# Optimization experiments

Measured on AMD Instinct MI355X. Metric: run time of the kernel, lower is better.

Reference implementation:

```python
import jax, jax.numpy as jnp
import numpy as np

LN_EPS = 1e-6


def setup_inputs() -> dict:
    key = jax.random.key(0)
    ks = jax.random.split(key, 10)
    B, S, D, M, P = 64, 512, 1024, 512, 3
    seq_out = jax.random.normal(ks[0], (B, S, D), dtype=jnp.float32)
    # dependency-tree style adjacency: sparse 0/1, stored dense as in the module
    adj = (jax.random.uniform(ks[1], (B, S, S)) < 0.02).astype(jnp.float32)
    aspect_mask = jax.random.randint(ks[2], (B, S), 0, 2, dtype=jnp.int32)
    # guarantee at least one aspect token per row (asp_wn divisor)
    aspect_mask = aspect_mask.at[:, 0].set(1)
    sc = 0.02
    return {
        "seq_out": seq_out,
        "adj": adj,
        "aspect_mask": aspect_mask,
        "ln_a": jnp.ones((D,), jnp.float32),
        "ln_b": jnp.zeros((D,), jnp.float32),
        "asp_w": jax.random.normal(ks[3], (D,), jnp.float32) * sc,
        "asp_b": jnp.zeros((), jnp.float32),
        "W0": jax.random.normal(ks[4], (D, M), jnp.float32) * sc,
        "b0": jnp.zeros((M,), jnp.float32),
        "W1": jax.random.normal(ks[5], (M, M), jnp.float32) * sc,
        "b1": jnp.zeros((M,), jnp.float32),
        "W2": jax.random.normal(ks[6], (M, M), jnp.float32) * sc,
        "b2": jnp.zeros((M,), jnp.float32),
        "cls_w": jax.random.normal(ks[7], (2 * M, P), jnp.float32) * sc,
        "cls_b": jnp.zeros((P,), jnp.float32),
    }


def _torch_layernorm(x, a, b):
    # torch code: a*(x-mean)/(std+eps)+b with unbiased std (Bessel, /(D-1))
    D = x.shape[-1]
    mean = jnp.mean(x, axis=-1, keepdims=True)
    xc = x - mean
    std = jnp.sqrt(jnp.sum(xc * xc, axis=-1, keepdims=True) / (D - 1))
    return a * xc / (std + LN_EPS) + b


def reference(seq_out, adj, aspect_mask, ln_a, ln_b, asp_w, asp_b,
              W0, b0, W1, b1, W2, b2, cls_w, cls_b):
    tgt = aspect_mask.astype(seq_out.dtype)                 # [B,S] labels == BCE weight (eval mode)
    x = _torch_layernorm(seq_out, ln_a, ln_b)               # [B,S,D]

    # aspect classification head + weighted BCEWithLogits (mean over all elems)
    z = jnp.einsum('bsd,d->bs', x, asp_w) + asp_b           # logits [B,S]
    bce = jnp.logaddexp(0.0, z) - z * tgt                   # stable BCE-with-logits
    loss_asp = jnp.mean(tgt * bce)
    aspect_pred = jax.nn.sigmoid(z)

    # dense-adjacency GCN (dropout = identity in eval)
    denom = jnp.sum(adj, axis=2, keepdims=True) + 1.0       # [B,S,1]
    out = x
    for W, b in ((W0, b0), (W1, b1), (W2, b2)):
        Ax = jnp.einsum('bst,btd->bsd', adj, out)           # aggregate
        out = jax.nn.relu((Ax @ W + b) / denom)             # project + degree-norm + relu

    # aspect-masked mean pool + global mean pool
    asp_wn = jnp.sum(tgt, axis=1, keepdims=True)            # [B,1]
    dep = jnp.einsum('bsm,bs->bm', out, tgt) / asp_wn       # [B,M]
    glob = jnp.mean(out, axis=1)                            # [B,M]

    feature = jnp.concatenate([dep, glob], axis=-1) @ cls_w + cls_b
    logits = jax.nn.softmax(feature, axis=1)
    return feature, logits, aspect_pred, loss_asp
```

## Files before the change

kernel.cpp:

```cpp
#include <hip/hip_runtime.h>
#include <math.h>

typedef __bf16 bf16;
typedef bf16 bf16x2 __attribute__((ext_vector_type(2)));
typedef bf16 bf16x4 __attribute__((ext_vector_type(4)));
typedef bf16 bf16x8 __attribute__((ext_vector_type(8)));
typedef float f32x4 __attribute__((ext_vector_type(4)));

#define NROWS 32768
#define DDIM 1024
#define MDIM 512

__device__ __forceinline__ float wave_reduce_sum(float v) {
#pragma unroll
  for (int o = 32; o > 0; o >>= 1) v += __shfl_down(v, o, 64);
  return v;
}
__device__ __forceinline__ float wave_allreduce_sum(float v) {
#pragma unroll
  for (int o = 32; o > 0; o >>= 1) v += __shfl_xor(v, o, 64);
  return v;
}

__device__ __forceinline__ void load_lds16(const bf16* g, bf16* l) {
  __builtin_amdgcn_global_load_lds(
      (const __attribute__((address_space(1))) unsigned int*)g,
      (__attribute__((address_space(3))) unsigned int*)l, 16, 0, 0);
}

__global__ __launch_bounds__(256) void prep_kernel(
    const float* __restrict__ seq, const float* __restrict__ adj,
    const int* __restrict__ amask, const float* __restrict__ ga,
    const float* __restrict__ gb, const float* __restrict__ aw,
    const float* __restrict__ ab, const float* __restrict__ W0,
    const float* __restrict__ W1, const float* __restrict__ W2,
    bf16* __restrict__ xn, float* __restrict__ aspect_pred,
    float* __restrict__ loss_arr, unsigned short* __restrict__ nbr,
    int* __restrict__ cnt, float* __restrict__ denomv,
    bf16* __restrict__ W0T, bf16* __restrict__ W1T, bf16* __restrict__ W2T) {
  const int bid = blockIdx.x;
  const int tid = threadIdx.x;
  const int lane = tid & 63;
  const int wv = tid >> 6;

  if (bid < 8192) {
    const int row = bid * 4 + wv;
    const float* xr = seq + (size_t)row * DDIM;
    float4 v[4];
    float s = 0.0f, sq = 0.0f;
#pragma unroll
    for (int j = 0; j < 4; ++j) {
      v[j] = *(const float4*)&xr[j * 256 + lane * 4];
      s += v[j].x + v[j].y + v[j].z + v[j].w;
      sq += v[j].x * v[j].x + v[j].y * v[j].y + v[j].z * v[j].z + v[j].w * v[j].w;
    }
    s = wave_allreduce_sum(s);
    sq = wave_allreduce_sum(sq);
    float mean = s * (1.0f / 1024.0f);
    float var = (sq - 1024.0f * mean * mean) * (1.0f / 1023.0f);
    var = fmaxf(var, 0.0f);
    float inv = 1.0f / (sqrtf(var) + 1e-6f);
    float zp = 0.0f;
#pragma unroll
    for (int j = 0; j < 4; ++j) {
      int c = j * 256 + lane * 4;
      float4 a4 = *(const float4*)&ga[c];
      float4 b4 = *(const float4*)&gb[c];
      float4 w4 = *(const float4*)&aw[c];
      float x0 = a4.x * (v[j].x - mean) * inv + b4.x;
      float x1 = a4.y * (v[j].y - mean) * inv + b4.y;
      float x2 = a4.z * (v[j].z - mean) * inv + b4.z;
      float x3 = a4.w * (v[j].w - mean) * inv + b4.w;
      bf16x4 o;
      o[0] = (bf16)x0; o[1] = (bf16)x1; o[2] = (bf16)x2; o[3] = (bf16)x3;
      *(bf16x4*)&xn[(size_t)row * DDIM + c] = o;
      zp += x0 * w4.x + x1 * w4.y + x2 * w4.z + x3 * w4.w;
    }
    zp = wave_reduce_sum(zp);
    if (lane == 0) {
      float z = zp + ab[0];
      aspect_pred[row] = 1.0f / (1.0f + expf(-z));
      float tgt = (float)amask[row];
      float bce = fmaxf(z, 0.0f) + log1pf(expf(-fabsf(z))) - z * tgt;
      loss_arr[row] = tgt * bce;
    }
  } else if (bid < 16384) {
    const int row = (bid - 8192) * 4 + wv;
    const float* ar = adj + (size_t)row * 512;
    unsigned short* nr = nbr + (size_t)row * 512;
    unsigned long long below = (1ull << lane) - 1ull;
    int base = 0;
#pragma unroll
    for (int t = 0; t < 2; ++t) {
      float4 v = *(const float4*)&ar[t * 256 + lane * 4];
      unsigned long long m0 = __ballot(v.x != 0.0f);
      unsigned long long m1 = __ballot(v.y != 0.0f);
      unsigned long long m2 = __ballot(v.z != 0.0f);
      unsigned long long m3 = __ballot(v.w != 0.0f);
      int c0 = __popcll(m0), c1 = __popcll(m1), c2 = __popcll(m2);
      int col = t * 256 + lane * 4;
      if (v.x != 0.0f) nr[base + __popcll(m0 & below)] = (unsigned short)(col + 0);
      if (v.y != 0.0f) nr[base + c0 + __popcll(m1 & below)] = (unsigned short)(col + 1);
      if (v.z != 0.0f) nr[base + c0 + c1 + __popcll(m2 & below)] = (unsigned short)(col + 2);
      if (v.w != 0.0f) nr[base + c0 + c1 + c2 + __popcll(m3 & below)] = (unsigned short)(col + 3);
      base += c0 + c1 + c2 + __popcll(m3);
    }
    if (lane == 0) { cnt[row] = base; denomv[row] = (float)base + 1.0f; }
  } else {
    int e = ((bid - 16384) * 256 + tid) * 4;
    if (e < 524288) {
      float4 v = *(const float4*)&W0[e];
      int k = e >> 9, n = e & 511;
      W0T[(size_t)(n + 0) * 1024 + k] = (bf16)v.x;
      W0T[(size_t)(n + 1) * 1024 + k] = (bf16)v.y;
      W0T[(size_t)(n + 2) * 1024 + k] = (bf16)v.z;
      W0T[(size_t)(n + 3) * 1024 + k] = (bf16)v.w;
    } else if (e < 786432) {
      int e2 = e - 524288;
      float4 v = *(const float4*)&W1[e2];
      int k = e2 >> 9, n = e2 & 511;
      W1T[(size_t)(n + 0) * 512 + k] = (bf16)v.x;
      W1T[(size_t)(n + 1) * 512 + k] = (bf16)v.y;
      W1T[(size_t)(n + 2) * 512 + k] = (bf16)v.z;
      W1T[(size_t)(n + 3) * 512 + k] = (bf16)v.w;
    } else {
      int e3 = e - 786432;
      float4 v = *(const float4*)&W2[e3];
      int k = e3 >> 9, n = e3 & 511;
      W2T[(size_t)(n + 0) * 512 + k] = (bf16)v.x;
      W2T[(size_t)(n + 1) * 512 + k] = (bf16)v.y;
      W2T[(size_t)(n + 2) * 512 + k] = (bf16)v.z;
      W2T[(size_t)(n + 3) * 512 + k] = (bf16)v.w;
    }
  }
}

#define BAR  __builtin_amdgcn_s_barrier()
#define WAITL do { asm volatile("s_waitcnt lgkmcnt(0)" ::: "memory"); \
                   __builtin_amdgcn_sched_barrier(0); } while (0)
#define WAITV4 do { asm volatile("s_waitcnt vmcnt(4)" ::: "memory"); \
                    __builtin_amdgcn_sched_barrier(0); } while (0)

__global__ __launch_bounds__(512, 2) void gemm256(const bf16* __restrict__ A,
                                                  const bf16* __restrict__ BT,
                                                  bf16* __restrict__ C,
                                                  int K) {
  __shared__ __align__(16) bf16 SMEM[65536];
  bf16 (*As)[16384] = (bf16(*)[16384])SMEM;
  bf16 (*Bs)[16384] = (bf16(*)[16384])(SMEM + 32768);
  const int tid = threadIdx.x;
  const int lane = tid & 63;
  const int wave = tid >> 6;
  const int wr = wave >> 2;
  const int wc = wave & 3;
  const int T = K >> 6;

  const int p = blockIdx.x;
  const int chunk = gridDim.x >> 3;
  const int wg = (p & 7) * chunk + (p >> 3);
  const int m0 = (wg >> 1) * 256;
  const int n0 = (wg & 1) * 256;

  const int srow = tid >> 3;
  const int scol8 = (tid & 7) ^ (srow & 7);

#define STAGEA(t, h)                                                          \
  do {                                                                        \
    int kt_ = ((t) < T) ? (t) * 64 : 0;                                       \
    const bf16* s_ = A + (size_t)(m0 + (h) * 128 + srow) * K + kt_ + scol8*8; \
    bf16* d_ = &As[(t) & 1][(h) * 8192 + wave * 512];                         \
    load_lds16(s_, d_);                                                       \
    load_lds16(s_ + (size_t)64 * K, d_ + 4096);                               \
  } while (0)
#define STAGEB(t, h)                                                          \
  do {                                                                        \
    int kt_ = ((t) < T) ? (t) * 64 : 0;                                       \
    const bf16* s_ = BT + (size_t)(n0 + (h) * 128 + srow) * K + kt_ + scol8*8;\
    bf16* d_ = &Bs[(t) & 1][(h) * 8192 + wave * 512];                         \
    load_lds16(s_, d_);                                                       \
    load_lds16(s_ + (size_t)64 * K, d_ + 4096);                               \
  } while (0)

  const int abase = (wr * 128 + (lane & 15)) * 64 + (lane >> 4) * 8;
  const int bbase = (wc * 64 + (lane & 15)) * 64 + (lane >> 4) * 8;
  const int axor = (lane & 7) << 3;

  bf16x8 areg[4][2], breg[4][2];
  f32x4 acc[8][4];
#pragma unroll
  for (int i = 0; i < 8; ++i)
#pragma unroll
    for (int j = 0; j < 4; ++j)
#pragma unroll
      for (int r = 0; r < 4; ++r) acc[i][j][r] = 0.0f;

#define LDA(buf_, qm)                                                         \
  _Pragma("unroll") for (int i_ = 0; i_ < 4; ++i_)                            \
  _Pragma("unroll") for (int h2_ = 0; h2_ < 2; ++h2_)                         \
    areg[i_][h2_] = *(const bf16x8*)&As[buf_][                                \
        (abase + ((qm)*4 + i_) * 1024 + h2_ * 32) ^ axor];
#define LDB(buf_, qn)                                                         \
  _Pragma("unroll") for (int j_ = 0; j_ < 2; ++j_)                            \
  _Pragma("unroll") for (int h2_ = 0; h2_ < 2; ++h2_)                         \
    breg[(qn)*2 + j_][h2_] = *(const bf16x8*)&Bs[buf_][                       \
        (bbase + ((qn)*2 + j_) * 1024 + h2_ * 32) ^ axor];
#define MFMAQ(qm, qn)                                                         \
  __builtin_amdgcn_s_setprio(1);                                              \
  _Pragma("unroll") for (int i_ = 0; i_ < 4; ++i_)                            \
  _Pragma("unroll") for (int j_ = 0; j_ < 2; ++j_)                            \
  _Pragma("unroll") for (int h2_ = 0; h2_ < 2; ++h2_)                         \
    acc[(qm)*4 + i_][(qn)*2 + j_] = __builtin_amdgcn_mfma_f32_16x16x32_bf16(  \
        areg[i_][h2_], breg[(qn)*2 + j_][h2_], acc[(qm)*4 + i_][(qn)*2 + j_], \
        0, 0, 0);                                                             \
  __builtin_amdgcn_s_setprio(0);

  STAGEA(0, 0); STAGEA(0, 1); STAGEB(0, 0); STAGEB(0, 1);
  STAGEB(1, 0); STAGEB(1, 1);
  WAITV4;
  BAR;

  const int NIT = T >> 1;
  for (int it = 0; it < NIT; ++it) {
    const int t1 = 2 * it + 1, t2 = 2 * it + 2, t3 = 2 * it + 3;
    LDA(0, 0); LDB(0, 0); STAGEA(t1, 0);
    BAR; WAITL; MFMAQ(0, 0); BAR;
    LDB(0, 1); STAGEA(t1, 1);
    BAR; WAITL; MFMAQ(0, 1); BAR;
    LDA(0, 1); STAGEB(t2, 0);
    BAR; WAITL; MFMAQ(1, 0); BAR;
    STAGEB(t2, 1);
    BAR; WAITL; MFMAQ(1, 1); WAITV4; BAR;
    LDA(1, 0); LDB(1, 0); STAGEA(t2, 0);
    BAR; WAITL; MFMAQ(0, 0); BAR;
    LDB(1, 1); STAGEA(t2, 1);
    BAR; WAITL; MFMAQ(0, 1); BAR;
    LDA(1, 1); STAGEB(t3, 0);
    BAR; WAITL; MFMAQ(1, 0); BAR;
    STAGEB(t3, 1);
    BAR; WAITL; MFMAQ(1, 1); WAITV4; BAR;
  }

  const int cn = lane & 15;
  const int rb = (lane >> 4) * 4;
#pragma unroll
  for (int i = 0; i < 8; ++i)
#pragma unroll
    for (int j = 0; j < 4; ++j) {
      int row = wr * 128 + i * 16 + rb;
      int colb = wc * 64 + j * 16 + cn;
#pragma unroll
      for (int r = 0; r < 4; ++r)
        SMEM[((row + r) << 8) + (colb ^ (((row + r) & 7) << 4))] =
            (bf16)acc[i][j][r];
    }
  __syncthreads();
  const size_t cbase = (size_t)m0 * MDIM + n0;
#pragma unroll
  for (int q = 0; q < 16; ++q) {
    int e = q * 4096 + tid * 8;
    int row = e >> 8, col = e & 255;
    *(bf16x8*)&C[cbase + (size_t)row * MDIM + col] =
        *(const bf16x8*)&SMEM[(row << 8) + (col ^ ((row & 7) << 4))];
  }
}

__global__ __launch_bounds__(128) void agg_kernel(const bf16* __restrict__ P,
                                                  const unsigned short* __restrict__ nbr,
                                                  const int* __restrict__ cnt,
                                                  const float* __restrict__ denomv,
                                                  const float* __restrict__ bias,
                                                  bf16* __restrict__ outb) {
  int p = blockIdx.x;
  int row = (p & 7) * 4096 + (p >> 3);
  int tid = threadIdx.x;
  int b = row >> 9;
  __shared__ unsigned short nl[512];
  int n = cnt[row];
  for (int i = tid; i < n; i += 128) nl[i] = nbr[(size_t)row * 512 + i];
  __syncthreads();
  const bf16* Pb = P + ((size_t)(b << 9)) * MDIM;
  int col = tid * 4;
  float a0 = 0, a1 = 0, a2 = 0, a3 = 0;
  for (int e = 0; e < n; ++e) {
    bf16x4 v = *(const bf16x4*)&Pb[(size_t)nl[e] * MDIM + col];
    a0 += (float)v[0]; a1 += (float)v[1]; a2 += (float)v[2]; a3 += (float)v[3];
  }
  float inv = 1.0f / denomv[row];
  float4 bb = *(const float4*)&bias[col];
  bf16x4 o;
  o[0] = (bf16)fmaxf((a0 + bb.x) * inv, 0.0f);
  o[1] = (bf16)fmaxf((a1 + bb.y) * inv, 0.0f);
  o[2] = (bf16)fmaxf((a2 + bb.z) * inv, 0.0f);
  o[3] = (bf16)fmaxf((a3 + bb.w) * inv, 0.0f);
  *(bf16x4*)&outb[(size_t)row * MDIM + col] = o;
}

__global__ __launch_bounds__(256) void pool_part(const bf16* __restrict__ outb,
                                                 const int* __restrict__ amask,
                                                 float* __restrict__ part) {
  int b = blockIdx.x >> 3;
  int slab = blockIdx.x & 7;
  int tid = threadIdx.x;
  int c0 = tid * 2;
  const bf16* ob = outb + (size_t)(b * 512 + slab * 64) * MDIM + c0;
  const int* am = amask + b * 512 + slab * 64;
  float a0 = 0, a1 = 0, t0 = 0, t1 = 0;
#pragma unroll 4
  for (int s = 0; s < 64; ++s) {
    bf16x2 v = *(const bf16x2*)&ob[(size_t)s * MDIM];
    float tg = (float)am[s];
    float v0 = (float)v[0], v1 = (float)v[1];
    a0 += v0; a1 += v1; t0 += v0 * tg; t1 += v1 * tg;
  }
  float* pp = part + ((size_t)blockIdx.x) * 1024;
  pp[c0] = t0; pp[c0 + 1] = t1;
  pp[512 + c0] = a0; pp[512 + c0 + 1] = a1;
}

__global__ __launch_bounds__(512) void poolcls_kernel(
    const float* __restrict__ part, const int* __restrict__ amask,
    const float* __restrict__ loss_arr, const float* __restrict__ cw,
    const float* __restrict__ cb, float* __restrict__ outp) {
  __shared__ float tg[512];
  __shared__ float shr[3][8];
  const int tid = threadIdx.x;
  const int b = blockIdx.x;

  if (b == 64) {
    float s = 0.0f;
    for (int i = tid; i < NROWS; i += 512) s += loss_arr[i];
    s = wave_reduce_sum(s);
    if ((tid & 63) == 0) shr[0][tid >> 6] = s;
    __syncthreads();
    if (tid == 0) {
      float t = 0.0f;
#pragma unroll
      for (int k = 0; k < 8; ++k) t += shr[0][k];
      outp[33152] = t * (1.0f / 32768.0f);
    }
    return;
  }

  tg[tid] = (float)amask[b * 512 + tid];
  __syncthreads();
  float wn = 0.0f;
#pragma unroll 8
  for (int s = 0; s < 512; ++s) wn += tg[s];
  float t = 0.0f, a = 0.0f;
  const float* pp = part + (size_t)b * 8 * 1024;
#pragma unroll
  for (int k = 0; k < 8; ++k) {
    t += pp[k * 1024 + tid];
    a += pp[k * 1024 + 512 + tid];
  }
  float f1 = t / wn;
  float f2 = a * (1.0f / 512.0f);

  float p0 = f1 * cw[tid * 3 + 0] + f2 * cw[(512 + tid) * 3 + 0];
  float p1 = f1 * cw[tid * 3 + 1] + f2 * cw[(512 + tid) * 3 + 1];
  float p2 = f1 * cw[tid * 3 + 2] + f2 * cw[(512 + tid) * 3 + 2];
  p0 = wave_reduce_sum(p0);
  p1 = wave_reduce_sum(p1);
  p2 = wave_reduce_sum(p2);
  if ((tid & 63) == 0) {
    shr[0][tid >> 6] = p0; shr[1][tid >> 6] = p1; shr[2][tid >> 6] = p2;
  }
  __syncthreads();
  if (tid == 0) {
    float q0 = 0, q1 = 0, q2 = 0;
#pragma unroll
    for (int k = 0; k < 8; ++k) { q0 += shr[0][k]; q1 += shr[1][k]; q2 += shr[2][k]; }
    q0 += cb[0]; q1 += cb[1]; q2 += cb[2];
    outp[b * 3 + 0] = q0;
    outp[b * 3 + 1] = q1;
    outp[b * 3 + 2] = q2;
    float m = fmaxf(q0, fmaxf(q1, q2));
    float e0 = expf(q0 - m), e1 = expf(q1 - m), e2 = expf(q2 - m);
    float inv = 1.0f / (e0 + e1 + e2);
    outp[192 + b * 3 + 0] = e0 * inv;
    outp[192 + b * 3 + 1] = e1 * inv;
    outp[192 + b * 3 + 2] = e2 * inv;
  }
}

extern "C" void kernel_launch(void* const* d_in, const int* in_sizes, int n_in,
                              void* d_out, int out_size, void* d_ws, size_t ws_size,
                              hipStream_t stream) {
  const float* seq   = (const float*)d_in[0];
  const float* adj   = (const float*)d_in[1];
  const int*   amask = (const int*)d_in[2];
  const float* ln_a  = (const float*)d_in[3];
  const float* ln_b  = (const float*)d_in[4];
  const float* asp_w = (const float*)d_in[5];
  const float* asp_b = (const float*)d_in[6];
  const float* W0    = (const float*)d_in[7];
  const float* b0    = (const float*)d_in[8];
  const float* W1    = (const float*)d_in[9];
  const float* b1    = (const float*)d_in[10];
  const float* W2    = (const float*)d_in[11];
  const float* b2    = (const float*)d_in[12];
  const float* cls_w = (const float*)d_in[13];
  const float* cls_b = (const float*)d_in[14];
  float* out = (float*)d_out;

  char* w = (char*)d_ws;
  bf16* P             = (bf16*)w;           w += (size_t)NROWS * MDIM * 2;
  bf16* xn            = (bf16*)w;           w += (size_t)NROWS * DDIM * 2;
  bf16* outb          = (bf16*)w;           w += (size_t)NROWS * MDIM * 2;
  unsigned short* nbr = (unsigned short*)w; w += (size_t)NROWS * 512 * 2;
  int* cnt            = (int*)w;            w += (size_t)NROWS * 4;
  float* denomv       = (float*)w;          w += (size_t)NROWS * 4;
  float* loss_arr     = (float*)w;          w += (size_t)NROWS * 4;
  float* part         = (float*)w;          w += (size_t)512 * 1024 * 4;
  bf16* W0T           = (bf16*)w;           w += (size_t)512 * 1024 * 2;
  bf16* W1T           = (bf16*)w;           w += (size_t)512 * 512 * 2;
  bf16* W2T           = (bf16*)w;           w += (size_t)512 * 512 * 2;

  prep_kernel<<<17408, 256, 0, stream>>>(seq, adj, amask, ln_a, ln_b, asp_w,
                                         asp_b, W0, W1, W2, xn, out + 384,
                                         loss_arr, nbr, cnt, denomv, W0T, W1T,
                                         W2T);
  gemm256<<<256, 512, 0, stream>>>(xn, W0T, P, 1024);
  agg_kernel<<<NROWS, 128, 0, stream>>>(P, nbr, cnt, denomv, b0, outb);
  gemm256<<<256, 512, 0, stream>>>(outb, W1T, P, 512);
  agg_kernel<<<NROWS, 128, 0, stream>>>(P, nbr, cnt, denomv, b1, outb);
  gemm256<<<256, 512, 0, stream>>>(outb, W2T, P, 512);
  agg_kernel<<<NROWS, 128, 0, stream>>>(P, nbr, cnt, denomv, b2, outb);
  pool_part<<<512, 256, 0, stream>>>(outb, amask, part);
  poolcls_kernel<<<65, 512, 0, stream>>>(part, amask, loss_arr, cls_w, cls_b,
                                         out);
}
```

Baseline: 266.0 us.

## Process eight rows per wave in prep kernel with prefetch; drop LDS staging in aggregation

```diff
diff --git a/kernel.cpp b/kernel.cpp
--- a/kernel.cpp
+++ b/kernel.cpp
@@ -43,94 +43,129 @@
   const int lane = tid & 63;
   const int wv = tid >> 6;
 
-  if (bid < 8192) {
-    const int row = bid * 4 + wv;
-    const float* xr = seq + (size_t)row * DDIM;
-    float4 v[4];
-    float s = 0.0f, sq = 0.0f;
-#pragma unroll
-    for (int j = 0; j < 4; ++j) {
-      v[j] = *(const float4*)&xr[j * 256 + lane * 4];
-      s += v[j].x + v[j].y + v[j].z + v[j].w;
-      sq += v[j].x * v[j].x + v[j].y * v[j].y + v[j].z * v[j].z + v[j].w * v[j].w;
-    }
-    s = wave_allreduce_sum(s);
-    sq = wave_allreduce_sum(sq);
-    float mean = s * (1.0f / 1024.0f);
-    float var = (sq - 1024.0f * mean * mean) * (1.0f / 1023.0f);
-    var = fmaxf(var, 0.0f);
-    float inv = 1.0f / (sqrtf(var) + 1e-6f);
-    float zp = 0.0f;
+  if (bid < 1024) {
+    const int row0 = (bid * 4 + wv) * 8;
+    float4 pa[4], pb[4], pw[4];
 #pragma unroll
     for (int j = 0; j < 4; ++j) {
       int c = j * 256 + lane * 4;
-      float4 a4 = *(const float4*)&ga[c];
-      float4 b4 = *(const float4*)&gb[c];
-      float4 w4 = *(const float4*)&aw[c];
-      float x0 = a4.x * (v[j].x - mean) * inv + b4.x;
-      float x1 = a4.y * (v[j].y - mean) * inv + b4.y;
-      float x2 = a4.z * (v[j].z - mean) * inv + b4.z;
-      float x3 = a4.w * (v[j].w - mean) * inv + b4.w;
-      bf16x4 o;
-      o[0] = (bf16)x0; o[1] = (bf16)x1; o[2] = (bf16)x2; o[3] = (bf16)x3;
-      *(bf16x4*)&xn[(size_t)row * DDIM + c] = o;
-      zp += x0 * w4.x + x1 * w4.y + x2 * w4.z + x3 * w4.w;
-    }
-    zp = wave_reduce_sum(zp);
-    if (lane == 0) {
-      float z = zp + ab[0];
-      aspect_pred[row] = 1.0f / (1.0f + expf(-z));
-      float tgt = (float)amask[row];
-      float bce = fmaxf(z, 0.0f) + log1pf(expf(-fabsf(z))) - z * tgt;
-      loss_arr[row] = tgt * bce;
-    }
-  } else if (bid < 16384) {
-    const int row = (bid - 8192) * 4 + wv;
-    const float* ar = adj + (size_t)row * 512;
-    unsigned short* nr = nbr + (size_t)row * 512;
-    unsigned long long below = (1ull << lane) - 1ull;
-    int base = 0;
-#pragma unroll
-    for (int t = 0; t < 2; ++t) {
-      float4 v = *(const float4*)&ar[t * 256 + lane * 4];
-      unsigned long long m0 = __ballot(v.x != 0.0f);
-      unsigned long long m1 = __ballot(v.y != 0.0f);
-      unsigned long long m2 = __ballot(v.z != 0.0f);
-      unsigned long long m3 = __ballot(v.w != 0.0f);
-      int c0 = __popcll(m0), c1 = __popcll(m1), c2 = __popcll(m2);
-      int col = t * 256 + lane * 4;
-      if (v.x != 0.0f) nr[base + __popcll(m0 & below)] = (unsigned short)(col + 0);
-      if (v.y != 0.0f) nr[base + c0 + __popcll(m1 & below)] = (unsigned short)(col + 1);
-      if (v.z != 0.0f) nr[base + c0 + c1 + __popcll(m2 & below)] = (unsigned short)(col + 2);
-      if (v.w != 0.0f) nr[base + c0 + c1 + c2 + __popcll(m3 & below)] = (unsigned short)(col + 3);
-      base += c0 + c1 + c2 + __popcll(m3);
-    }
-    if (lane == 0) { cnt[row] = base; denomv[row] = (float)base + 1.0f; }
+      pa[j] = *(const float4*)&ga[c];
+      pb[j] = *(const float4*)&gb[c];
+      pw[j] = *(const float4*)&aw[c];
+    }
+    const float ab0 = ab[0];
+    float4 v[4], vn[4];
+    {
+      const float* xr = seq + (size_t)row0 * DDIM;
+#pragma unroll
+      for (int j = 0; j < 4; ++j) vn[j] = *(const float4*)&xr[j * 256 + lane * 4];
+    }
+    for (int i = 0; i < 8; ++i) {
+      const int row = row0 + i;
+#pragma unroll
+      for (int j = 0; j < 4; ++j) v[j] = vn[j];
+      if (i < 7) {
+        const float* xr = seq + (size_t)(row + 1) * DDIM;
+#pragma unroll
+        for (int j = 0; j < 4; ++j) vn[j] = *(const float4*)&xr[j * 256 + lane * 4];
+      }
+      float s = 0.0f, sq = 0.0f;
+#pragma unroll
+      for (int j = 0; j < 4; ++j) {
+        s += v[j].x + v[j].y + v[j].z + v[j].w;
+        sq += v[j].x * v[j].x + v[j].y * v[j].y + v[j].z * v[j].z + v[j].w * v[j].w;
+      }
+      s = wave_allreduce_sum(s);
+      sq = wave_allreduce_sum(sq);
+      float mean = s * (1.0f / 1024.0f);
+      float var = (sq - 1024.0f * mean * mean) * (1.0f / 1023.0f);
+      var = fmaxf(var, 0.0f);
+      float inv = 1.0f / (sqrtf(var) + 1e-6f);
+      float zp = 0.0f;
+#pragma unroll
+      for (int j = 0; j < 4; ++j) {
+        float x0 = pa[j].x * (v[j].x - mean) * inv + pb[j].x;
+        float x1 = pa[j].y * (v[j].y - mean) * inv + pb[j].y;
+        float x2 = pa[j].z * (v[j].z - mean) * inv + pb[j].z;
+        float x3 = pa[j].w * (v[j].w - mean) * inv + pb[j].w;
+        bf16x4 o;
+        o[0] = (bf16)x0; o[1] = (bf16)x1; o[2] = (bf16)x2; o[3] = (bf16)x3;
+        *(bf16x4*)&xn[(size_t)row * DDIM + j * 256 + lane * 4] = o;
+        zp += x0 * pw[j].x + x1 * pw[j].y + x2 * pw[j].z + x3 * pw[j].w;
+      }
+      zp = wave_reduce_sum(zp);
+      if (lane == 0) {
+        float z = zp + ab0;
+        aspect_pred[row] = 1.0f / (1.0f + expf(-z));
+        float tgt = (float)amask[row];
+        float bce = fmaxf(z, 0.0f) + log1pf(expf(-fabsf(z))) - z * tgt;
+        loss_arr[row] = tgt * bce;
+      }
+    }
+  } else if (bid < 2048) {
+    const int row0 = ((bid - 1024) * 4 + wv) * 8;
+    const unsigned long long below = (1ull << lane) - 1ull;
+    float4 a0, a1, a0n, a1n;
+    {
+      const float* ar = adj + (size_t)row0 * 512;
+      a0n = *(const float4*)&ar[lane * 4];
+      a1n = *(const float4*)&ar[256 + lane * 4];
+    }
+    for (int i = 0; i < 8; ++i) {
+      const int row = row0 + i;
+      a0 = a0n; a1 = a1n;
+      if (i < 7) {
+        const float* ar = adj + (size_t)(row + 1) * 512;
+        a0n = *(const float4*)&ar[lane * 4];
+        a1n = *(const float4*)&ar[256 + lane * 4];
+      }
+      unsigned short* nr = nbr + (size_t)row * 512;
+      int base = 0;
+#pragma unroll
+      for (int t = 0; t < 2; ++t) {
+        float4 vv = t ? a1 : a0;
+        unsigned long long m0 = __ballot(vv.x != 0.0f);
+        unsigned long long m1 = __ballot(vv.y != 0.0f);
+        unsigned long long m2 = __ballot(vv.z != 0.0f);
+        unsigned long long m3 = __ballot(vv.w != 0.0f);
+        int c0 = __popcll(m0), c1 = __popcll(m1), c2 = __popcll(m2);
+        int col = t * 256 + lane * 4;
+        if (vv.x != 0.0f) nr[base + __popcll(m0 & below)] = (unsigned short)(col + 0);
+        if (vv.y != 0.0f) nr[base + c0 + __popcll(m1 & below)] = (unsigned short)(col + 1);
+        if (vv.z != 0.0f) nr[base + c0 + c1 + __popcll(m2 & below)] = (unsigned short)(col + 2);
+        if (vv.w != 0.0f) nr[base + c0 + c1 + c2 + __popcll(m3 & below)] = (unsigned short)(col + 3);
+        base += c0 + c1 + c2 + __popcll(m3);
+      }
+      if (lane == 0) { cnt[row] = base; denomv[row] = (float)base + 1.0f; }
+    }
   } else {
-    int e = ((bid - 16384) * 256 + tid) * 4;
-    if (e < 524288) {
-      float4 v = *(const float4*)&W0[e];
-      int k = e >> 9, n = e & 511;
-      W0T[(size_t)(n + 0) * 1024 + k] = (bf16)v.x;
-      W0T[(size_t)(n + 1) * 1024 + k] = (bf16)v.y;
-      W0T[(size_t)(n + 2) * 1024 + k] = (bf16)v.z;
-      W0T[(size_t)(n + 3) * 1024 + k] = (bf16)v.w;
-    } else if (e < 786432) {
-      int e2 = e - 524288;
-      float4 v = *(const float4*)&W1[e2];
-      int k = e2 >> 9, n = e2 & 511;
-      W1T[(size_t)(n + 0) * 512 + k] = (bf16)v.x;
-      W1T[(size_t)(n + 1) * 512 + k] = (bf16)v.y;
-      W1T[(size_t)(n + 2) * 512 + k] = (bf16)v.z;
-      W1T[(size_t)(n + 3) * 512 + k] = (bf16)v.w;
-    } else {
-      int e3 = e - 786432;
-      float4 v = *(const float4*)&W2[e3];
-      int k = e3 >> 9, n = e3 & 511;
-      W2T[(size_t)(n + 0) * 512 + k] = (bf16)v.x;
-      W2T[(size_t)(n + 1) * 512 + k] = (bf16)v.y;
-      W2T[(size_t)(n + 2) * 512 + k] = (bf16)v.z;
-      W2T[(size_t)(n + 3) * 512 + k] = (bf16)v.w;
+    const int idx = (bid - 2048) * 256 + tid;
+    for (int e4 = idx; e4 < 262144; e4 += 32768) {
+      int e = e4 * 4;
+      if (e < 524288) {
+        float4 v = *(const float4*)&W0[e];
+        int k = e >> 9, n = e & 511;
+        W0T[(size_t)(n + 0) * 1024 + k] = (bf16)v.x;
+        W0T[(size_t)(n + 1) * 1024 + k] = (bf16)v.y;
+        W0T[(size_t)(n + 2) * 1024 + k] = (bf16)v.z;
+        W0T[(size_t)(n + 3) * 1024 + k] = (bf16)v.w;
+      } else if (e < 786432) {
+        int e2 = e - 524288;
+        float4 v = *(const float4*)&W1[e2];
+        int k = e2 >> 9, n = e2 & 511;
+        W1T[(size_t)(n + 0) * 512 + k] = (bf16)v.x;
+        W1T[(size_t)(n + 1) * 512 + k] = (bf16)v.y;
+        W1T[(size_t)(n + 2) * 512 + k] = (bf16)v.z;
+        W1T[(size_t)(n + 3) * 512 + k] = (bf16)v.w;
+      } else {
+        int e3 = e - 786432;
+        float4 v = *(const float4*)&W2[e3];
+        int k = e3 >> 9, n = e3 & 511;
+        W2T[(size_t)(n + 0) * 512 + k] = (bf16)v.x;
+        W2T[(size_t)(n + 1) * 512 + k] = (bf16)v.y;
+        W2T[(size_t)(n + 2) * 512 + k] = (bf16)v.z;
+        W2T[(size_t)(n + 3) * 512 + k] = (bf16)v.w;
+      }
     }
   }
 }
@@ -274,15 +309,14 @@
   int row = (p & 7) * 4096 + (p >> 3);
   int tid = threadIdx.x;
   int b = row >> 9;
-  __shared__ unsigned short nl[512];
   int n = cnt[row];
-  for (int i = tid; i < n; i += 128) nl[i] = nbr[(size_t)row * 512 + i];
-  __syncthreads();
+  const unsigned short* nr = nbr + (size_t)row * 512;
   const bf16* Pb = P + ((size_t)(b << 9)) * MDIM;
   int col = tid * 4;
   float a0 = 0, a1 = 0, a2 = 0, a3 = 0;
   for (int e = 0; e < n; ++e) {
-    bf16x4 v = *(const bf16x4*)&Pb[(size_t)nl[e] * MDIM + col];
+    int idx = nr[e];
+    bf16x4 v = *(const bf16x4*)&Pb[(size_t)idx * MDIM + col];
     a0 += (float)v[0]; a1 += (float)v[1]; a2 += (float)v[2]; a3 += (float)v[3];
   }
   float inv = 1.0f / denomv[row];
@@ -416,10 +450,10 @@
   bf16* W1T           = (bf16*)w;           w += (size_t)512 * 512 * 2;
   bf16* W2T           = (bf16*)w;           w += (size_t)512 * 512 * 2;
 
-  prep_kernel<<<17408, 256, 0, stream>>>(seq, adj, amask, ln_a, ln_b, asp_w,
-                                         asp_b, W0, W1, W2, xn, out + 384,
-                                         loss_arr, nbr, cnt, denomv, W0T, W1T,
-                                         W2T);
+  prep_kernel<<<2176, 256, 0, stream>>>(seq, adj, amask, ln_a, ln_b, asp_w,
+                                        asp_b, W0, W1, W2, xn, out + 384,
+                                        loss_arr, nbr, cnt, denomv, W0T, W1T,
+                                        W2T);
   gemm256<<<256, 512, 0, stream>>>(xn, W0T, P, 1024);
   agg_kernel<<<NROWS, 128, 0, stream>>>(P, nbr, cnt, denomv, b0, outb);
   gemm256<<<256, 512, 0, stream>>>(outb, W1T, P, 512);
```

After: 331.9 us. +24.8%, slower.
